# Performance work log

Measured on AMD Instinct MI355X. Metric: run time of the kernel, lower is better.

Reference implementation:

```python
import jax, jax.numpy as jnp
import numpy as np
import math

B, S, D = 4, 4096, 256


def setup_inputs() -> dict:
    key = jax.random.key(0)
    ks = jax.random.split(key, 9)
    s = 1.0 / math.sqrt(D)
    return {
        "src": jax.random.normal(ks[0], (B, S, D), dtype=jnp.float32),
        "Wq": jax.random.normal(ks[1], (D, D), dtype=jnp.float32) * s,
        "bq": jax.random.normal(ks[2], (D,), dtype=jnp.float32) * s,
        "Wk": jax.random.normal(ks[3], (D, D), dtype=jnp.float32) * s,
        "bk": jax.random.normal(ks[4], (D,), dtype=jnp.float32) * s,
        "Wv": jax.random.normal(ks[5], (D, D), dtype=jnp.float32) * s,
        "bv": jax.random.normal(ks[6], (D,), dtype=jnp.float32) * s,
        "Wo": jax.random.normal(ks[7], (D, D), dtype=jnp.float32) * s,
        "bo": jax.random.normal(ks[8], (D,), dtype=jnp.float32) * s,
    }


def reference(src, Wq, bq, Wk, bk, Wv, bv, Wo, bo):
    # Linear layers (torch Linear: x @ W.T + b)
    q = src @ Wq.T + bq  # [B,S,D]
    k = src @ Wk.T + bk
    v = src @ Wv.T + bv

    # Pad mask is built from the TRANSFORMED q/k, channel 0 != 0.
    # After (mask_q*mask_k).transpose(1,2): mask[b,i,j] = (q[b,i,0]!=0)&(k[b,i,0]!=0)
    # -> depends only on the row index i; broadcast over j.
    row_mask = (q[:, :, 0] != 0) & (k[:, :, 0] != 0)  # [B,S]
    mask = row_mask[:, :, None]  # [B,S,1] broadcast over keys

    scale = 1.0 / math.sqrt(D)
    scores = jnp.einsum("bid,bjd->bij", q, k) * scale  # [B,S,S]
    scores = jnp.where(mask, scores, jnp.float32(-1e9))
    prob = jax.nn.softmax(scores, axis=-1)
    prob = jnp.where(mask, prob, 0.0)
    out = jnp.einsum("bij,bjd->bid", prob, v)  # [B,S,D]
    return out @ Wo.T + bo
```

## Files before the change

kernel.cpp:

```cpp
#include <hip/hip_runtime.h>


typedef __bf16 bf16x8 __attribute__((ext_vector_type(8)));
typedef float  f32x4  __attribute__((ext_vector_type(4)));

__device__ __forceinline__ f32x4 mfma16(bf16x8 a, bf16x8 b, f32x4 c) {
  return __builtin_amdgcn_mfma_f32_16x16x32_bf16(a, b, c, 0, 0, 0);
}

__device__ __forceinline__ unsigned pack2(float a, float b) {
  unsigned ua = __builtin_bit_cast(unsigned, a);
  unsigned ub = __builtin_bit_cast(unsigned, b);
  ua += 0x7fffu + ((ua >> 16) & 1u);
  ub += 0x7fffu + ((ub >> 16) & 1u);
  return (ua >> 16) | (ub & 0xffff0000u);
}

__device__ __forceinline__ float bfu(unsigned short u) {
  unsigned v = (unsigned)u << 16;
  return __builtin_bit_cast(float, v);
}

typedef __attribute__((address_space(1))) void gas_void;
typedef __attribute__((address_space(3))) void las_void;
__device__ __forceinline__ void gl2lds16(const void* g, void* l) {
  __builtin_amdgcn_global_load_lds((gas_void*)g, (las_void*)l, 16, 0, 0);
}

__global__ __launch_bounds__(256) void cvt_kernel(const float* __restrict__ src,
                                                  const float* __restrict__ Wq,
                                                  const float* __restrict__ Wk,
                                                  const float* __restrict__ Wv,
                                                  const float* __restrict__ Wo,
                                                  __bf16* __restrict__ Sb,
                                                  __bf16* __restrict__ Wb) {
  size_t e = ((size_t)blockIdx.x * 256 + threadIdx.x) * 8;
  const float* sp;
  __bf16* dp;
  if (e < 4194304) {
    sp = src + e;
    dp = Sb + e;
  } else {
    size_t f = e - 4194304;
    int w = (int)(f >> 16);
    size_t off = f & 65535;
    sp = (w == 0 ? Wq : w == 1 ? Wk : w == 2 ? Wv : Wo) + off;
    dp = Wb + ((size_t)w << 16) + off;
  }
  float4 a = ((const float4*)sp)[0], b2 = ((const float4*)sp)[1];
  uint4 o;
  o.x = pack2(a.x, a.y);  o.y = pack2(a.z, a.w);
  o.z = pack2(b2.x, b2.y); o.w = pack2(b2.z, b2.w);
  *(uint4*)dp = o;
}

__global__ __launch_bounds__(256) void qkv_kernel(const __bf16* __restrict__ Sb,
                                                  const __bf16* __restrict__ Wb,
                                                  const float* __restrict__ bq,
                                                  const float* __restrict__ bk,
                                                  const float* __restrict__ bv,
                                                  __bf16* __restrict__ Qb,
                                                  __bf16* __restrict__ Kb,
                                                  __bf16* __restrict__ Vt) {
  __shared__ __align__(16) char smem[65536];
  const int mb = blockIdx.x, nb = blockIdx.y;
  const __bf16* Wsel = Wb + (size_t)(nb < 2 ? 0 : (nb < 4 ? 1 : 2)) * 65536;
  const float* bias = nb < 2 ? bq : (nb < 4 ? bk : bv);
  __bf16* Y = nb < 2 ? Qb : (nb < 4 ? Kb : Vt);
  const int nn = nb & 1;
  const int tid = threadIdx.x, wid = tid >> 6, lane = tid & 63;
  const int l15 = lane & 15, hi = lane >> 4;
  const int wm = wid & 1, wn = wid >> 1;

  const int srow_off = lane >> 3;
  const int ssu = (lane & 7) ^ srow_off;

  const __bf16* Xg = Sb + (size_t)(mb * 128) * 256;
  const __bf16* Wg = Wsel + (size_t)(nn * 128) * 256;

  f32x4 acc[4][4] = {};

  auto stage = [&](int t, int p) {
    char* xd = smem + p * 32768;
    char* wd = xd + 16384;
#pragma unroll
    for (int i = 0; i < 4; i++) {
      int row = wid * 32 + i * 8 + srow_off;
      gl2lds16(Xg + (size_t)row * 256 + t * 64 + ssu * 8, xd + (wid * 4 + i) * 1024);
      gl2lds16(Wg + (size_t)row * 256 + t * 64 + ssu * 8, wd + (wid * 4 + i) * 1024);
    }
  };

  stage(0, 0);
  __syncthreads();

  for (int t = 0; t < 4; t++) {
    const int p = t & 1;
    if (t + 1 < 4) stage(t + 1, p ^ 1);
    const char* xb = smem + p * 32768;
    const char* wbuf = xb + 16384;
#pragma unroll
    for (int kk = 0; kk < 2; kk++) {
      const int sp16 = ((kk * 4 + hi) ^ (l15 & 7)) * 16;
      bf16x8 wf[4], xf[4];
#pragma unroll
      for (int i = 0; i < 4; i++) {
        wf[i] = *(const bf16x8*)(wbuf + (wn * 64 + i * 16 + l15) * 128 + sp16);
        xf[i] = *(const bf16x8*)(xb + (wm * 64 + i * 16 + l15) * 128 + sp16);
      }
      if (nb < 4) {
#pragma unroll
        for (int i = 0; i < 4; i++)
#pragma unroll
          for (int j = 0; j < 4; j++) acc[i][j] = mfma16(wf[i], xf[j], acc[i][j]);
      } else {
#pragma unroll
        for (int i = 0; i < 4; i++)
#pragma unroll
          for (int j = 0; j < 4; j++) acc[i][j] = mfma16(xf[i], wf[j], acc[i][j]);
      }
    }
    __syncthreads();
  }

  if (nb < 4) {
#pragma unroll
    for (int i = 0; i < 4; i++)
#pragma unroll
      for (int j = 0; j < 4; j++) {
        int m  = mb * 128 + wm * 64 + j * 16 + l15;
        int n0 = nn * 128 + wn * 64 + i * 16 + hi * 4;
        float4 bb = *(const float4*)&bias[n0];
        f32x4 a = acc[i][j];
        uint2 w; w.x = pack2(a[0] + bb.x, a[1] + bb.y); w.y = pack2(a[2] + bb.z, a[3] + bb.w);
        *(uint2*)(Y + (size_t)m * 256 + n0) = w;
      }
  } else {
#pragma unroll
    for (int i = 0; i < 4; i++)
#pragma unroll
      for (int j = 0; j < 4; j++) {
        int mg = mb * 128 + wm * 64 + i * 16 + hi * 4;
        int n  = nn * 128 + wn * 64 + j * 16 + l15;
        int b_ = mg >> 12, s = mg & 4095;
        float bn = bias[n];
        f32x4 a = acc[i][j];
        uint2 w; w.x = pack2(a[0] + bn, a[1] + bn); w.y = pack2(a[2] + bn, a[3] + bn);
        *(uint2*)(Y + ((size_t)(b_ * 256 + n)) * 4096 + s) = w;
      }
  }
}

__global__ __launch_bounds__(256, 2) void attn_kernel(const __bf16* __restrict__ Qb,
                                                      const __bf16* __restrict__ Kb,
                                                      const __bf16* __restrict__ Vt,
                                                      __bf16* __restrict__ Op,
                                                      float* __restrict__ Lp) {
  __shared__ __align__(16) char smem[65536];
  const int bid = blockIdx.x;
  const int pair = bid & 15, slot = bid >> 4;
  const int b = pair >> 2, ck = pair & 3;
  const int tid = threadIdx.x, wid = tid >> 6, lane = tid & 63;
  const int l15 = lane & 15, hi = lane >> 4;
  const int grow0 = b * 4096 + slot * 128 + wid * 32;
  const int key00 = ck * 1024;

  const char* KbaseB = (const char*)Kb + (size_t)b * 4096 * 512;
  const char* VbaseB = (const char*)Vt + (size_t)b * 256 * 8192;

  bf16x8 qf[2][8];
#pragma unroll
  for (int g = 0; g < 2; g++) {
    const __bf16* qrow = Qb + (size_t)(grow0 + g * 16 + l15) * 256 + hi * 8;
#pragma unroll
    for (int c8 = 0; c8 < 8; c8++) qf[g][c8] = *(const bf16x8*)(qrow + c8 * 32);
  }

  f32x4 oacc[2][16] = {};
  float lsum[2] = {0.f, 0.f};
  bf16x8 pfc0, pfc1;

  auto stageK = [&](int t, int p) {
    char* kd = smem + p * 16384;
    const char* kg = KbaseB + (size_t)(key00 + t * 32) * 512;
#pragma unroll
    for (int i = 0; i < 4; i++) {
      int chk = wid * 4 + i;
      int r = chk * 2 + (lane >> 5);
      int su = (lane & 31) ^ (r & 31);
      gl2lds16(kg + r * 512 + su * 16, kd + chk * 1024);
    }
  };
  auto stageV = [&](int t, int p) {
    char* vd = smem + 32768 + p * 16384;
    const char* vg = VbaseB + (size_t)(key00 + t * 32) * 2;
#pragma unroll
    for (int i = 0; i < 4; i++) {
      int chk = wid * 4 + i;
      int L = chk * 8 + (lane >> 3);
      int su = (lane & 7) ^ (L & 7);
      int d = 2 * L + (su >> 2);
      gl2lds16(vg + (size_t)d * 8192 + (su & 3) * 16, vd + chk * 1024);
    }
  };

  auto qk = [&](int p, f32x4& s00, f32x4& s01, f32x4& s10, f32x4& s11) {
    const char* kb = smem + p * 16384;
#pragma unroll
    for (int c8 = 0; c8 < 8; c8++) {
      int sp0 = ((c8 * 4 + hi) ^ l15) << 4;
      bf16x8 k0 = *(const bf16x8*)(kb + l15 * 512 + sp0);
      bf16x8 k1 = *(const bf16x8*)(kb + (16 + l15) * 512 + (sp0 ^ 256));
      s00 = mfma16(k0, qf[0][c8], s00);
      s01 = mfma16(k0, qf[1][c8], s01);
      s10 = mfma16(k1, qf[0][c8], s10);
      s11 = mfma16(k1, qf[1][c8], s11);
    }
  };

  auto softmax = [&](f32x4 s00, f32x4 s01, f32x4 s10, f32x4 s11) {
#pragma unroll
    for (int g = 0; g < 2; g++) {
      const f32x4 sa = g ? s01 : s00;
      const f32x4 sb = g ? s11 : s10;
      float p0[4], p1[4];
#pragma unroll
      for (int r = 0; r < 4; r++) {
        p0[r] = __expf(sa[r] * 0.0625f);
        p1[r] = __expf(sb[r] * 0.0625f);
      }
      lsum[g] += (p0[0] + p0[1]) + (p0[2] + p0[3]) + (p1[0] + p1[1]) + (p1[2] + p1[3]);

      unsigned pk00 = pack2(p0[0], p0[1]);
      unsigned pk01 = pack2(p0[2], p0[3]);
      unsigned pk10 = pack2(p1[0], p1[1]);
      unsigned pk11 = pack2(p1[2], p1[3]);
      int srcA = ((hi & 1) << 5) | l15;
      int srcB = srcA + 16;
      unsigned A0 = (unsigned)__shfl((int)pk00, srcA);
      unsigned A1 = (unsigned)__shfl((int)pk01, srcA);
      unsigned C0 = (unsigned)__shfl((int)pk10, srcA);
      unsigned C1 = (unsigned)__shfl((int)pk11, srcA);
      unsigned B0 = (unsigned)__shfl((int)pk00, srcB);
      unsigned B1 = (unsigned)__shfl((int)pk01, srcB);
      unsigned D0 = (unsigned)__shfl((int)pk10, srcB);
      unsigned D1 = (unsigned)__shfl((int)pk11, srcB);
      bool sel = hi >= 2;
      union { unsigned u[4]; bf16x8 v; } un;
      un.u[0] = sel ? C0 : A0;
      un.u[1] = sel ? C1 : A1;
      un.u[2] = sel ? D0 : B0;
      un.u[3] = sel ? D1 : B1;
      if (g == 0) pfc0 = un.v; else pfc1 = un.v;
    }
  };

  stageK(0, 0);
  stageV(0, 0);
  __syncthreads();
  {
    f32x4 s00{}, s01{}, s10{}, s11{};
    qk(0, s00, s01, s10, s11);
    stageK(1, 1);
    softmax(s00, s01, s10, s11);
  }
  __syncthreads();

  for (int t = 0; t < 32; t++) {
    if (t + 2 < 32) stageK(t + 2, t & 1);
    if (t + 1 < 32) stageV(t + 1, (t + 1) & 1);

    f32x4 s00{}, s01{}, s10{}, s11{};
    __builtin_amdgcn_s_setprio(1);
    if (t + 1 < 32) qk((t + 1) & 1, s00, s01, s10, s11);

    const char* vb = smem + 32768 + (t & 1) * 16384;
#pragma unroll
    for (int tt = 0; tt < 16; tt++) {
      int L = tt * 8 + (l15 >> 1);
      int su = (((l15 & 1) << 2) + hi) ^ (L & 7);
      bf16x8 vf = *(const bf16x8*)(vb + L * 128 + (su << 4));
      oacc[0][tt] = mfma16(vf, pfc0, oacc[0][tt]);
      oacc[1][tt] = mfma16(vf, pfc1, oacc[1][tt]);
    }
    __builtin_amdgcn_s_setprio(0);

    if (t + 1 < 32) softmax(s00, s01, s10, s11);
    __syncthreads();
  }

#pragma unroll
  for (int g = 0; g < 2; g++) {
    float ls = lsum[g];
    ls += __shfl_xor(ls, 16);
    ls += __shfl_xor(ls, 32);
    const int grow = grow0 + g * 16 + l15;
    if (hi == 0) Lp[ck * 16384 + grow] = ls;

    __bf16* orow = Op + ((size_t)ck * 16384 + grow) * 256;
#pragma unroll
    for (int tt = 0; tt < 16; tt++) {
      int d0 = tt * 16 + (hi << 2);
      f32x4 a = oacc[g][tt];
      uint2 w; w.x = pack2(a[0], a[1]); w.y = pack2(a[2], a[3]);
      *(uint2*)(orow + d0) = w;
    }
  }
}

__global__ __launch_bounds__(256) void combine_kernel(const __bf16* __restrict__ Op,
                                                      const float* __restrict__ Lp,
                                                      const __bf16* __restrict__ Qb,
                                                      const __bf16* __restrict__ Kb,
                                                      __bf16* __restrict__ Ob) {
  const int idx = blockIdx.x * 256 + threadIdx.x;
  const int row = idx >> 5;
  const int d0 = (idx & 31) << 3;
  float l = Lp[row] + Lp[16384 + row] + Lp[32768 + row] + Lp[49152 + row];
  float m = ((float)Qb[(size_t)row * 256] != 0.f && (float)Kb[(size_t)row * 256] != 0.f)
                ? 1.f : 0.f;
  float inv = m / l;
  float a[8] = {};
#pragma unroll
  for (int c = 0; c < 4; c++) {
    uint4 u = *(const uint4*)(Op + ((size_t)c * 16384 + row) * 256 + d0);
    const unsigned short* us = (const unsigned short*)&u;
#pragma unroll
    for (int j = 0; j < 8; j++) a[j] += bfu(us[j]);
  }
  uint4 o;
  o.x = pack2(a[0] * inv, a[1] * inv);
  o.y = pack2(a[2] * inv, a[3] * inv);
  o.z = pack2(a[4] * inv, a[5] * inv);
  o.w = pack2(a[6] * inv, a[7] * inv);
  *(uint4*)(Ob + (size_t)row * 256 + d0) = o;
}

__global__ __launch_bounds__(256) void out_proj_kernel(const __bf16* __restrict__ Ob,
                                                       const __bf16* __restrict__ Wb3,
                                                       const float* __restrict__ bias,
                                                       float* __restrict__ out) {
  __shared__ __align__(16) char smem[49152];
  const int mb = blockIdx.x, nb = blockIdx.y;
  const int tid = threadIdx.x, wid = tid >> 6, lane = tid & 63;
  const int l15 = lane & 15, hi = lane >> 4;
  const int srow_off = lane >> 3;
  const int ssu = (lane & 7) ^ srow_off;

  const __bf16* Xg = Ob + (size_t)(mb * 64) * 256;
  const __bf16* Wg = Wb3 + (size_t)(nb * 128) * 256;

  f32x4 acc[2][4] = {};

  auto stage = [&](int t, int p) {
    char* xd = smem + p * 24576;
    char* wd = xd + 8192;
#pragma unroll
    for (int i = 0; i < 2; i++) {
      int row = wid * 16 + i * 8 + srow_off;
      gl2lds16(Xg + (size_t)row * 256 + t * 64 + ssu * 8, xd + (wid * 2 + i) * 1024);
    }
#pragma unroll
    for (int i = 0; i < 4; i++) {
      int row = wid * 32 + i * 8 + srow_off;
      gl2lds16(Wg + (size_t)row * 256 + t * 64 + ssu * 8, wd + (wid * 4 + i) * 1024);
    }
  };

  stage(0, 0);
  __syncthreads();

  for (int t = 0; t < 4; t++) {
    const int p = t & 1;
    if (t + 1 < 4) stage(t + 1, p ^ 1);
    const char* xb = smem + p * 24576;
    const char* wbuf = xb + 8192;
#pragma unroll
    for (int kk = 0; kk < 2; kk++) {
      const int sp16 = ((kk * 4 + hi) ^ (l15 & 7)) * 16;
      bf16x8 wf[2], xf[4];
#pragma unroll
      for (int i = 0; i < 2; i++)
        wf[i] = *(const bf16x8*)(wbuf + (wid * 32 + i * 16 + l15) * 128 + sp16);
#pragma unroll
      for (int j = 0; j < 4; j++)
        xf[j] = *(const bf16x8*)(xb + (j * 16 + l15) * 128 + sp16);
#pragma unroll
      for (int i = 0; i < 2; i++)
#pragma unroll
        for (int j = 0; j < 4; j++) acc[i][j] = mfma16(wf[i], xf[j], acc[i][j]);
    }
    __syncthreads();
  }

#pragma unroll
  for (int i = 0; i < 2; i++)
#pragma unroll
    for (int j = 0; j < 4; j++) {
      int m  = mb * 64 + j * 16 + l15;
      int n0 = nb * 128 + wid * 32 + i * 16 + hi * 4;
      float4 bb = *(const float4*)&bias[n0];
      f32x4 a = acc[i][j];
      float4 o; o.x = a[0] + bb.x; o.y = a[1] + bb.y; o.z = a[2] + bb.z; o.w = a[3] + bb.w;
      *(float4*)(out + (size_t)m * 256 + n0) = o;
    }
}

extern "C" void kernel_launch(void* const* d_in, const int* in_sizes, int n_in,
                              void* d_out, int out_size, void* d_ws, size_t ws_size,
                              hipStream_t stream) {
  const float* src = (const float*)d_in[0];
  const float* Wq  = (const float*)d_in[1];
  const float* bq  = (const float*)d_in[2];
  const float* Wk  = (const float*)d_in[3];
  const float* bk  = (const float*)d_in[4];
  const float* Wv  = (const float*)d_in[5];
  const float* bv  = (const float*)d_in[6];
  const float* Wo  = (const float*)d_in[7];
  const float* bo  = (const float*)d_in[8];
  float* out = (float*)d_out;

  char* ws = (char*)d_ws;
  __bf16* Sb = (__bf16*)(ws);
  __bf16* Wb = (__bf16*)(ws + (8u << 20));
  __bf16* Qb = (__bf16*)(ws + (10u << 20));
  __bf16* Kb = (__bf16*)(ws + (18u << 20));
  __bf16* Vt = (__bf16*)(ws + (26u << 20));
  __bf16* Op = (__bf16*)(ws + (34u << 20));
  float*  Lp = (float*)(ws + (66u << 20));
  __bf16* Ob = (__bf16*)(ws + (66u << 20) + (1u << 18));

  cvt_kernel<<<2176, 256, 0, stream>>>(src, Wq, Wk, Wv, Wo, Sb, Wb);
  qkv_kernel<<<dim3(128, 6), 256, 0, stream>>>(Sb, Wb, bq, bk, bv, Qb, Kb, Vt);
  attn_kernel<<<512, 256, 0, stream>>>(Qb, Kb, Vt, Op, Lp);
  combine_kernel<<<2048, 256, 0, stream>>>(Op, Lp, Qb, Kb, Ob);
  out_proj_kernel<<<dim3(256, 2), 256, 0, stream>>>(Ob, Wb + 3 * 65536, bo, out);
}
```

Measured before the change: 214.8 us.

## Pipeline attention loop with explicit vmcnt waits and split QK/PV stages

Replaces __syncthreads in the flash-attention main loop with raw s_barrier plus targeted s_waitcnt vmcnt counts. Global-to-LDS K/V loads can then stay in flight across barriers instead of being fully drained each step. The loop is reordered so QK and softmax for the next tile run before the PV product of the current tile, using double-buffered probability fragments. The last two iterations are peeled out. The risk is that the hand-counted vmcnt values and buffer indices must match the outstanding loads exactly, or LDS reads race with the async copies.

```diff
diff --git a/kernel.cpp b/kernel.cpp
--- a/kernel.cpp
+++ b/kernel.cpp
@@ -26,6 +26,13 @@
 __device__ __forceinline__ void gl2lds16(const void* g, void* l) {
   __builtin_amdgcn_global_load_lds((gas_void*)g, (las_void*)l, 16, 0, 0);
 }
+
+#define WAITV(n) asm volatile("s_waitcnt vmcnt(" #n ")" ::: "memory")
+#define BARRIER()                         \
+  do {                                    \
+    __builtin_amdgcn_s_barrier();         \
+    __builtin_amdgcn_sched_barrier(0);    \
+  } while (0)
 
 __global__ __launch_bounds__(256) void cvt_kernel(const float* __restrict__ src,
                                                   const float* __restrict__ Wq,
@@ -178,7 +185,7 @@
 
   f32x4 oacc[2][16] = {};
   float lsum[2] = {0.f, 0.f};
-  bf16x8 pfc0, pfc1;
+  bf16x8 pfA0, pfA1, pfB0, pfB1;
 
   auto stageK = [&](int t, int p) {
     char* kd = smem + p * 16384;
@@ -206,6 +213,7 @@
 
   auto qk = [&](int p, f32x4& s00, f32x4& s01, f32x4& s10, f32x4& s11) {
     const char* kb = smem + p * 16384;
+    __builtin_amdgcn_s_setprio(1);
 #pragma unroll
     for (int c8 = 0; c8 < 8; c8++) {
       int sp0 = ((c8 * 4 + hi) ^ l15) << 4;
@@ -216,9 +224,11 @@
       s10 = mfma16(k1, qf[0][c8], s10);
       s11 = mfma16(k1, qf[1][c8], s11);
     }
-  };
-
-  auto softmax = [&](f32x4 s00, f32x4 s01, f32x4 s10, f32x4 s11) {
+    __builtin_amdgcn_s_setprio(0);
+  };
+
+  auto softmax = [&](const f32x4& s00, const f32x4& s01, const f32x4& s10,
+                     const f32x4& s11, bf16x8& o0, bf16x8& o1) {
 #pragma unroll
     for (int g = 0; g < 2; g++) {
       const f32x4 sa = g ? s01 : s00;
@@ -251,43 +261,64 @@
       un.u[1] = sel ? C1 : A1;
       un.u[2] = sel ? D0 : B0;
       un.u[3] = sel ? D1 : B1;
-      if (g == 0) pfc0 = un.v; else pfc1 = un.v;
-    }
-  };
-
-  stageK(0, 0);
-  stageV(0, 0);
-  __syncthreads();
-  {
-    f32x4 s00{}, s01{}, s10{}, s11{};
-    qk(0, s00, s01, s10, s11);
-    stageK(1, 1);
-    softmax(s00, s01, s10, s11);
-  }
-  __syncthreads();
-
-  for (int t = 0; t < 32; t++) {
-    if (t + 2 < 32) stageK(t + 2, t & 1);
-    if (t + 1 < 32) stageV(t + 1, (t + 1) & 1);
-
-    f32x4 s00{}, s01{}, s10{}, s11{};
+      if (g == 0) o0 = un.v; else o1 = un.v;
+    }
+  };
+
+  auto pv = [&](int p, bf16x8 f0, bf16x8 f1) {
+    const char* vb = smem + 32768 + p * 16384;
     __builtin_amdgcn_s_setprio(1);
-    if (t + 1 < 32) qk((t + 1) & 1, s00, s01, s10, s11);
-
-    const char* vb = smem + 32768 + (t & 1) * 16384;
 #pragma unroll
     for (int tt = 0; tt < 16; tt++) {
       int L = tt * 8 + (l15 >> 1);
       int su = (((l15 & 1) << 2) + hi) ^ (L & 7);
       bf16x8 vf = *(const bf16x8*)(vb + L * 128 + (su << 4));
-      oacc[0][tt] = mfma16(vf, pfc0, oacc[0][tt]);
-      oacc[1][tt] = mfma16(vf, pfc1, oacc[1][tt]);
+      oacc[0][tt] = mfma16(vf, f0, oacc[0][tt]);
+      oacc[1][tt] = mfma16(vf, f1, oacc[1][tt]);
     }
     __builtin_amdgcn_s_setprio(0);
-
-    if (t + 1 < 32) softmax(s00, s01, s10, s11);
-    __syncthreads();
-  }
+  };
+
+  stageK(0, 0);
+  stageK(1, 1);
+  stageV(0, 0);
+  WAITV(8);
+  BARRIER();
+  {
+    f32x4 s00{}, s01{}, s10{}, s11{};
+    qk(0, s00, s01, s10, s11);
+    softmax(s00, s01, s10, s11, pfA0, pfA1);
+  }
+  BARRIER();
+
+  for (int t = 0; t < 30; t++) {
+    stageK(t + 2, t & 1);
+    WAITV(8);
+    BARRIER();
+    stageV(t + 1, (t + 1) & 1);
+    f32x4 s00{}, s01{}, s10{}, s11{};
+    qk((t + 1) & 1, s00, s01, s10, s11);
+    softmax(s00, s01, s10, s11, pfB0, pfB1);
+    WAITV(8);
+    BARRIER();
+    pv(t & 1, pfA0, pfA1);
+    pfA0 = pfB0; pfA1 = pfB1;
+  }
+  {
+    WAITV(4);
+    BARRIER();
+    stageV(31, 1);
+    f32x4 s00{}, s01{}, s10{}, s11{};
+    qk(1, s00, s01, s10, s11);
+    softmax(s00, s01, s10, s11, pfB0, pfB1);
+    WAITV(4);
+    BARRIER();
+    pv(0, pfA0, pfA1);
+    pfA0 = pfB0; pfA1 = pfB1;
+  }
+  WAITV(0);
+  BARRIER();
+  pv(1, pfA0, pfA1);
 
 #pragma unroll
   for (int g = 0; g < 2; g++) {
```

New measurement: 220.3 us. 1.03x slower.
